# Kernel optimization log

Measured on AMD Instinct MI355X. Metric: run time of the kernel, lower is better.

## Reference

```python
import jax, jax.numpy as jnp
import numpy as np

# --- SOM geometry constants (match init_kwargs) ---
MAP_ROWS, MAP_COLS = 32, 32
N_PROTO = MAP_ROWS * MAP_COLS
SIGMA = 1.0
PBC = True


def _build_neighborhood():
    """Gaussian neighborhood h[i,j]=exp(-dist(i,j)^2/(2*sigma^2)) on a hexagonal
    grid with periodic boundary conditions (faithful to Neighborhoods(...,'Hexagons','grid',PBC=True))."""
    rr, cc = np.meshgrid(np.arange(MAP_ROWS), np.arange(MAP_COLS), indexing='ij')
    # hexagonal lattice coordinates: odd rows shifted by 0.5, row spacing sqrt(3)/2
    x = cc + 0.5 * (rr % 2)
    y = rr * (np.sqrt(3.0) / 2.0)
    pos = np.stack([x.ravel(), y.ravel()], axis=1).astype(np.float64)  # [M, 2]
    diff = pos[:, None, :] - pos[None, :, :]                            # [M, M, 2]
    if PBC:
        width = float(MAP_COLS)
        height = MAP_ROWS * (np.sqrt(3.0) / 2.0)
        d2 = np.full((N_PROTO, N_PROTO), np.inf)
        for sx in (-1.0, 0.0, 1.0):
            for sy in (-1.0, 0.0, 1.0):
                dx = diff[..., 0] + sx * width
                dy = diff[..., 1] + sy * height
                d2 = np.minimum(d2, dx * dx + dy * dy)
    else:
        d2 = (diff ** 2).sum(-1)
    return np.exp(-d2 / (2.0 * SIGMA ** 2)).astype(np.float32)         # [M, M]


H = jnp.asarray(_build_neighborhood())  # constant [M, M] neighborhood matrix


def setup_inputs() -> dict:
    key = jax.random.key(0)
    k1, k2 = jax.random.split(key)
    inputs = jax.random.normal(k1, (16384, 256), dtype=jnp.float32)
    prototypes = jax.random.normal(k2, (N_PROTO, 256), dtype=jnp.float32) * 0.05
    return {"inputs": inputs, "prototypes": prototypes}


def reference(inputs, prototypes):
    # squared euclidean distances d[n, m] = ||x_n - p_m||^2, computed without
    # materializing the (N, M, D) broadcast intermediate
    x2 = jnp.sum(inputs * inputs, axis=1, keepdims=True)        # [N, 1]
    p2 = jnp.sum(prototypes * prototypes, axis=1)               # [M]
    d = x2 - 2.0 * (inputs @ prototypes.T) + p2[None, :]        # [N, M]
    energies = H @ d.T                                          # [M, N]
    bmus = jnp.argmin(energies, axis=0)                         # [N]
    out = 0.5 * jnp.take_along_axis(energies, bmus[None, :], axis=0)  # [1, N]
    return out
```

## Files before the change

### kernel.cpp

```cpp
#include <hip/hip_runtime.h>
#include <hip/hip_bf16.h>
#include <math.h>

#define D 256
#define NPROTO 1024
#define WR 13
#define WC 18
#define WJ (WR * WC)
#define JSUB 59
#define GMAT_BLOCKS (NPROTO / 4)
#define XPREP_BLOCKS (16384 / 8)

#define WAITVM(N) asm volatile("s_waitcnt vmcnt(" #N ")" ::: "memory")

typedef __attribute__((ext_vector_type(8))) short short8;
typedef __attribute__((ext_vector_type(4))) short s16x4;
typedef __attribute__((ext_vector_type(4))) float f32x4;

__device__ __forceinline__ short f2bf(float f) {
    union { __hip_bfloat16 b; short s; } u;
    u.b = __float2bfloat16(f);
    return u.s;
}

__device__ __forceinline__ void gload_lds16(void* lds, const void* g) {
    __builtin_amdgcn_global_load_lds(
        (const __attribute__((address_space(1))) unsigned*)g,
        (__attribute__((address_space(3))) unsigned*)lds, 16, 0, 0);
}

__device__ __forceinline__ void proto_pos(int idx, double& x, double& y) {
    int r = idx >> 5, c = idx & 31;
    x = (double)c + 0.5 * (double)(r & 1);
    y = (double)r * 0.86602540378443864676;
}

__device__ __forceinline__ float hval(int i, int j) {
    double xi, yi, xj, yj;
    proto_pos(i, xi, yi);
    proto_pos(j, xj, yj);
    double dx0 = xi - xj, dy0 = yi - yj;
    const double W = 32.0;
    const double Hh = 27.712812921102035;
    double best = 1e300;
#pragma unroll
    for (int sx = -1; sx <= 1; ++sx) {
        double dx = dx0 + (double)sx * W;
#pragma unroll
        for (int sy = -1; sy <= 1; ++sy) {
            double dy = dy0 + (double)sy * Hh;
            double d2 = dx * dx + dy * dy;
            best = fmin(best, d2);
        }
    }
    return (float)exp(-0.5 * best);
}

__global__ void __launch_bounds__(256) prep_kernel(
    const float* __restrict__ X, const float* __restrict__ P,
    short* __restrict__ Xg, short* __restrict__ Gb,
    float* __restrict__ x2, float* __restrict__ hsum, float* __restrict__ hp2,
    unsigned* __restrict__ out) {
    int t = threadIdx.x;
    int bx = blockIdx.x;

    if (bx >= GMAT_BLOCKS) {
        int row = (bx - GMAT_BLOCKS) * 8 + (t >> 5);
        int g = t & 31;
        const float4* src = reinterpret_cast<const float4*>(X + (size_t)row * D) + g * 2;
        float4 a = src[0], b = src[1];
        float s = a.x * a.x + a.y * a.y + a.z * a.z + a.w * a.w +
                  b.x * b.x + b.y * b.y + b.z * b.z + b.w * b.w;
        s += __shfl_xor(s, 1);
        s += __shfl_xor(s, 2);
        s += __shfl_xor(s, 4);
        s += __shfl_xor(s, 8);
        s += __shfl_xor(s, 16);
        if (g == 0) x2[row] = s;
        short8 w;
        w[0] = f2bf(a.x); w[1] = f2bf(a.y); w[2] = f2bf(a.z); w[3] = f2bf(a.w);
        w[4] = f2bf(b.x); w[5] = f2bf(b.y); w[6] = f2bf(b.z); w[7] = f2bf(b.w);
        int sw = ((g * 8) & 63) ^ ((row & 7) << 3);
        *reinterpret_cast<short8*>(Xg + (size_t)row * D + ((g >> 3) << 6) + sw) = w;
        if (t < 8) out[(bx - GMAT_BLOCKS) * 8 + t] = 0x7f800000u;
        return;
    }

    __shared__ float ht[4][WJ];
    __shared__ int jrow[WJ];
    __shared__ __align__(16) float gpart[4][4][256];
    __shared__ float hqred[4][4];
    __shared__ float hsred[4][4];
    int i0 = bx * 4;
    int r0 = i0 >> 5, c0 = i0 & 31;

    for (int u = t; u < WJ; u += 256) {
        int jr = (r0 + (u / WC) - 6 + 32) & 31;
        int jc = (c0 + (u % WC) - 7 + 32) & 31;
        int j = jr * 32 + jc;
        jrow[u] = j;
#pragma unroll
        for (int s = 0; s < 4; ++s) ht[s][u] = hval(i0 + s, j);
    }
    __syncthreads();

    int w = t >> 6, lane = t & 63;
    int j0 = w * JSUB;
    int j1 = (j0 + JSUB < WJ) ? j0 + JSUB : WJ;
    f32x4 g[4] = {{0.f, 0.f, 0.f, 0.f}, {0.f, 0.f, 0.f, 0.f},
                  {0.f, 0.f, 0.f, 0.f}, {0.f, 0.f, 0.f, 0.f}};
    float hqp[4] = {0.f, 0.f, 0.f, 0.f};
    float hsp[4] = {0.f, 0.f, 0.f, 0.f};
    for (int u = j0; u < j1; ++u) {
        f32x4 pv = *reinterpret_cast<const f32x4*>(P + (size_t)jrow[u] * D + lane * 4);
        float q = pv[0] * pv[0] + pv[1] * pv[1] + pv[2] * pv[2] + pv[3] * pv[3];
#pragma unroll
        for (int s = 0; s < 4; ++s) {
            float h = ht[s][u];
            g[s][0] = fmaf(h, pv[0], g[s][0]);
            g[s][1] = fmaf(h, pv[1], g[s][1]);
            g[s][2] = fmaf(h, pv[2], g[s][2]);
            g[s][3] = fmaf(h, pv[3], g[s][3]);
            hqp[s] = fmaf(h, q, hqp[s]);
            hsp[s] += h;
        }
    }
#pragma unroll
    for (int s = 0; s < 4; ++s)
        *reinterpret_cast<f32x4*>(&gpart[w][s][lane * 4]) = g[s];
#pragma unroll
    for (int s = 0; s < 4; ++s) {
#pragma unroll
        for (int off = 1; off < 64; off <<= 1) hqp[s] += __shfl_xor(hqp[s], off);
    }
    if (lane == 0) {
#pragma unroll
        for (int s = 0; s < 4; ++s) { hqred[w][s] = hqp[s]; hsred[w][s] = hsp[s]; }
    }
    __syncthreads();

    {
        int s = t >> 6;
        f32x4 gs = *reinterpret_cast<const f32x4*>(&gpart[0][s][lane * 4]);
#pragma unroll
        for (int ww = 1; ww < 4; ++ww) {
            f32x4 gp = *reinterpret_cast<const f32x4*>(&gpart[ww][s][lane * 4]);
            gs[0] += gp[0]; gs[1] += gp[1]; gs[2] += gp[2]; gs[3] += gp[3];
        }
        int i = i0 + s;
        s16x4 wv = {f2bf(gs[0]), f2bf(gs[1]), f2bf(gs[2]), f2bf(gs[3])};
        int sw = ((lane * 4) & 63) ^ ((i & 7) << 3);
        *reinterpret_cast<s16x4*>(Gb + (size_t)i * D + ((lane >> 4) << 6) + sw) = wv;
    }
    if (t < 4) {
        hsum[i0 + t] = hsred[0][t] + hsred[1][t] + hsred[2][t] + hsred[3][t];
    } else if (t < 8) {
        int s = t - 4;
        hp2[i0 + s] = hqred[0][s] + hqred[1][s] + hqred[2][s] + hqred[3][s];
    }
}

__global__ void __launch_bounds__(256, 2) som5_kernel(
    const short* __restrict__ Xg, const short* __restrict__ Gb,
    const float* __restrict__ x2, const float* __restrict__ hsum,
    const float* __restrict__ hp2, unsigned* __restrict__ out) {
    __shared__ __align__(16) short Xs[2][128 * 64];
    __shared__ __align__(16) short Gs[2][128 * 64];
    __shared__ float red[2][128];

    const int t = threadIdx.x;
    const int lane = t & 63;
    const int wid = t >> 6;
    const int wr = wid >> 1;
    const int wc = wid & 1;
    const int lm = lane & 15;
    const int lq = lane >> 4;
    const int n0 = blockIdx.x * 128;
    const int ib0 = blockIdx.y * 256;

    f32x4 acc[2][4][4];
#pragma unroll
    for (int it = 0; it < 2; ++it)
#pragma unroll
        for (int m = 0; m < 4; ++m)
#pragma unroll
            for (int n = 0; n < 4; ++n) acc[it][m][n] = (f32x4){0.f, 0.f, 0.f, 0.f};

    auto stage_X = [&](int xb, int kt) {
#pragma unroll
        for (int q = 0; q < 4; ++q) {
            int row = q * 32 + (t >> 3);
            gload_lds16((char*)(&Xs[xb][0]) + q * 4096 + t * 16,
                        Xg + (size_t)(n0 + row) * D + kt * 64 + (t & 7) * 8);
        }
    };
    auto stage_G = [&](int gb, int kt, int it) {
#pragma unroll
        for (int q = 0; q < 4; ++q) {
            int row = q * 32 + (t >> 3);
            gload_lds16((char*)(&Gs[gb][0]) + q * 4096 + t * 16,
                        Gb + (size_t)(ib0 + it * 128 + row) * D + kt * 64 + (t & 7) * 8);
        }
    };

    auto compute = [&](int xb, int gb, int it) {
#pragma unroll
        for (int kk = 0; kk < 2; ++kk) {
            const int off = (kk * 32 + lq * 8) ^ ((lm & 7) << 3);
            short8 a[4], b[4];
#pragma unroll
            for (int m = 0; m < 4; ++m)
                a[m] = *reinterpret_cast<const short8*>(
                    &Xs[xb][(wr * 64 + m * 16 + lm) * 64 + off]);
#pragma unroll
            for (int n = 0; n < 4; ++n)
                b[n] = *reinterpret_cast<const short8*>(
                    &Gs[gb][(wc * 64 + n * 16 + lm) * 64 + off]);
            __builtin_amdgcn_s_setprio(1);
#pragma unroll
            for (int m = 0; m < 4; ++m)
#pragma unroll
                for (int n = 0; n < 4; ++n)
                    acc[it][m][n] = __builtin_amdgcn_mfma_f32_16x16x32_bf16(a[m], b[n], acc[it][m][n], 0, 0, 0);
            __builtin_amdgcn_s_setprio(0);
        }
    };

    stage_G(0, 0, 0);
    stage_X(0, 0);

#pragma unroll
    for (int p = 0; p < 8; ++p) {
        if (p < 7) {
            const int pn = p + 1, ktn = pn >> 1, itn = pn & 1;
            if (itn == 0) stage_X(ktn & 1, ktn);
            stage_G(pn & 1, ktn, itn);
        }
        if (p == 7) { WAITVM(0); }
        else if (p & 1) { WAITVM(8); }
        else { WAITVM(4); }
        __builtin_amdgcn_sched_barrier(0);
        __builtin_amdgcn_s_barrier();
        compute((p >> 1) & 1, p & 1, p & 1);
        __builtin_amdgcn_s_barrier();
    }

    float x2v[4][4];
#pragma unroll
    for (int m = 0; m < 4; ++m)
#pragma unroll
        for (int j = 0; j < 4; ++j)
            x2v[m][j] = x2[n0 + wr * 64 + m * 16 + lq * 4 + j];

    float rmin[4][4];
#pragma unroll
    for (int m = 0; m < 4; ++m)
#pragma unroll
        for (int j = 0; j < 4; ++j) rmin[m][j] = 3.4e38f;

#pragma unroll
    for (int it = 0; it < 2; ++it)
#pragma unroll
        for (int ni = 0; ni < 4; ++ni) {
            int ig = ib0 + it * 128 + wc * 64 + ni * 16 + lm;
            float hs = hsum[ig];
            float hq = hp2[ig];
#pragma unroll
            for (int m = 0; m < 4; ++m)
#pragma unroll
                for (int j = 0; j < 4; ++j) {
                    float e = fmaf(hs, x2v[m][j], hq) - 2.0f * acc[it][m][ni][j];
                    rmin[m][j] = fminf(rmin[m][j], e);
                }
        }

#pragma unroll
    for (int m = 0; m < 4; ++m)
#pragma unroll
        for (int j = 0; j < 4; ++j) {
            float v = rmin[m][j];
            v = fminf(v, __shfl_xor(v, 1));
            v = fminf(v, __shfl_xor(v, 2));
            v = fminf(v, __shfl_xor(v, 4));
            v = fminf(v, __shfl_xor(v, 8));
            rmin[m][j] = v;
        }
    if (lm == 0) {
#pragma unroll
        for (int m = 0; m < 4; ++m)
#pragma unroll
            for (int j = 0; j < 4; ++j)
                red[wc][wr * 64 + m * 16 + lq * 4 + j] = rmin[m][j];
    }
    __syncthreads();
    if (t < 128) {
        float v = fminf(red[0][t], red[1][t]);
        atomicMin(out + n0 + t, __float_as_uint(0.5f * v));
    }
}

extern "C" void kernel_launch(void* const* d_in, const int* in_sizes, int n_in,
                              void* d_out, int out_size, void* d_ws, size_t ws_size,
                              hipStream_t stream) {
    const float* X = (const float*)d_in[0];
    const float* P = (const float*)d_in[1];
    unsigned* out = (unsigned*)d_out;
    int N = in_sizes[0] / D;

    float* ws = (float*)d_ws;
    float* hsum = ws + 1024;
    float* hp2 = ws + 2048;
    float* x2 = ws + 4096;
    short* Gb = (short*)(ws + 32768);
    short* Xg = (short*)(ws + 262144);

    prep_kernel<<<GMAT_BLOCKS + XPREP_BLOCKS, 256, 0, stream>>>(
        X, P, Xg, Gb, x2, hsum, hp2, out);
    som5_kernel<<<dim3(N / 128, NPROTO / 256), 256, 0, stream>>>(
        Xg, Gb, x2, hsum, hp2, out);
}
```

Baseline: 31.97 us.

## Pre-swizzle G into MFMA fragment layout and load B operands directly from global

The prep kernel now writes the bf16 G matrix in a fragment-ordered layout, so each lane can load its MFMA B operand with one 16-byte global load. The main kernel drops the G LDS staging buffer and reads B fragments straight into registers, staging only X through LDS. Each block now covers 128 prototypes instead of 256, which halves the accumulators and doubles the grid. The aim is to cut LDS traffic and barriers and raise occupancy, at the cost of reloading X twice as often across blocks and relying on global-load latency being hidden by the vmcnt waits.

```diff
diff --git a/kernel.cpp b/kernel.cpp
--- a/kernel.cpp
+++ b/kernel.cpp
@@ -14,7 +14,6 @@
 #define WAITVM(N) asm volatile("s_waitcnt vmcnt(" #N ")" ::: "memory")
 
 typedef __attribute__((ext_vector_type(8))) short short8;
-typedef __attribute__((ext_vector_type(4))) short s16x4;
 typedef __attribute__((ext_vector_type(4))) float f32x4;
 
 __device__ __forceinline__ short f2bf(float f) {
@@ -58,7 +57,7 @@
 
 __global__ void __launch_bounds__(256) prep_kernel(
     const float* __restrict__ X, const float* __restrict__ P,
-    short* __restrict__ Xg, short* __restrict__ Gb,
+    short* __restrict__ Xg, short* __restrict__ GbF,
     float* __restrict__ x2, float* __restrict__ hsum, float* __restrict__ hp2,
     unsigned* __restrict__ out) {
     int t = threadIdx.x;
@@ -147,10 +146,22 @@
             f32x4 gp = *reinterpret_cast<const f32x4*>(&gpart[ww][s][lane * 4]);
             gs[0] += gp[0]; gs[1] += gp[1]; gs[2] += gp[2]; gs[3] += gp[3];
         }
-        int i = i0 + s;
-        s16x4 wv = {f2bf(gs[0]), f2bf(gs[1]), f2bf(gs[2]), f2bf(gs[3])};
-        int sw = ((lane * 4) & 63) ^ ((i & 7) << 3);
-        *reinterpret_cast<s16x4*>(Gb + (size_t)i * D + ((lane >> 4) << 6) + sw) = wv;
+        float h0 = __shfl_down(gs[0], 1);
+        float h1 = __shfl_down(gs[1], 1);
+        float h2 = __shfl_down(gs[2], 1);
+        float h3 = __shfl_down(gs[3], 1);
+        if (!(lane & 1)) {
+            int c = lane >> 1;
+            int kg = c >> 2;
+            int q = c & 3;
+            int i = i0 + s;
+            int Ig = i >> 4;
+            short8 wv;
+            wv[0] = f2bf(gs[0]); wv[1] = f2bf(gs[1]); wv[2] = f2bf(gs[2]); wv[3] = f2bf(gs[3]);
+            wv[4] = f2bf(h0);    wv[5] = f2bf(h1);    wv[6] = f2bf(h2);    wv[7] = f2bf(h3);
+            *reinterpret_cast<short8*>(
+                GbF + ((size_t)(Ig * 8 + kg) << 9) + ((i & 15) + 16 * q) * 8) = wv;
+        }
     }
     if (t < 4) {
         hsum[i0 + t] = hsred[0][t] + hsred[1][t] + hsred[2][t] + hsred[3][t];
@@ -160,12 +171,11 @@
     }
 }
 
-__global__ void __launch_bounds__(256, 2) som5_kernel(
-    const short* __restrict__ Xg, const short* __restrict__ Gb,
+__global__ void __launch_bounds__(256) som7_kernel(
+    const short* __restrict__ Xg, const short* __restrict__ GbF,
     const float* __restrict__ x2, const float* __restrict__ hsum,
     const float* __restrict__ hp2, unsigned* __restrict__ out) {
     __shared__ __align__(16) short Xs[2][128 * 64];
-    __shared__ __align__(16) short Gs[2][128 * 64];
     __shared__ float red[2][128];
 
     const int t = threadIdx.x;
@@ -176,15 +186,14 @@
     const int lm = lane & 15;
     const int lq = lane >> 4;
     const int n0 = blockIdx.x * 128;
-    const int ib0 = blockIdx.y * 256;
-
-    f32x4 acc[2][4][4];
-#pragma unroll
-    for (int it = 0; it < 2; ++it)
-#pragma unroll
-        for (int m = 0; m < 4; ++m)
-#pragma unroll
-            for (int n = 0; n < 4; ++n) acc[it][m][n] = (f32x4){0.f, 0.f, 0.f, 0.f};
+    const int ib0 = blockIdx.y * 128;
+    const int Igbase = (ib0 >> 4) + wc * 4;
+
+    f32x4 acc[4][4];
+#pragma unroll
+    for (int m = 0; m < 4; ++m)
+#pragma unroll
+        for (int n = 0; n < 4; ++n) acc[m][n] = (f32x4){0.f, 0.f, 0.f, 0.f};
 
     auto stage_X = [&](int xb, int kt) {
 #pragma unroll
@@ -194,55 +203,57 @@
                         Xg + (size_t)(n0 + row) * D + kt * 64 + (t & 7) * 8);
         }
     };
-    auto stage_G = [&](int gb, int kt, int it) {
-#pragma unroll
-        for (int q = 0; q < 4; ++q) {
-            int row = q * 32 + (t >> 3);
-            gload_lds16((char*)(&Gs[gb][0]) + q * 4096 + t * 16,
-                        Gb + (size_t)(ib0 + it * 128 + row) * D + kt * 64 + (t & 7) * 8);
-        }
-    };
-
-    auto compute = [&](int xb, int gb, int it) {
-#pragma unroll
-        for (int kk = 0; kk < 2; ++kk) {
-            const int off = (kk * 32 + lq * 8) ^ ((lm & 7) << 3);
-            short8 a[4], b[4];
+
+    stage_X(0, 0);
+
+#pragma unroll
+    for (int kt = 0; kt < 4; ++kt) {
+        short8 b0[4], b1[4];
+#pragma unroll
+        for (int n = 0; n < 4; ++n) {
+            const short* fb = GbF + ((size_t)((Igbase + n) * 8 + kt * 2) << 9) + lane * 8;
+            b0[n] = *reinterpret_cast<const short8*>(fb);
+            b1[n] = *reinterpret_cast<const short8*>(fb + 512);
+        }
+        __builtin_amdgcn_sched_barrier(0);
+        if (kt < 3) stage_X((kt + 1) & 1, kt + 1);
+        if (kt < 3) { WAITVM(12); } else { WAITVM(8); }
+        __builtin_amdgcn_sched_barrier(0);
+        __builtin_amdgcn_s_barrier();
+
+        const short* xb = &Xs[kt & 1][0];
+        {
+            const int off = (lq * 8) ^ ((lm & 7) << 3);
+            short8 a[4];
 #pragma unroll
             for (int m = 0; m < 4; ++m)
                 a[m] = *reinterpret_cast<const short8*>(
-                    &Xs[xb][(wr * 64 + m * 16 + lm) * 64 + off]);
-#pragma unroll
-            for (int n = 0; n < 4; ++n)
-                b[n] = *reinterpret_cast<const short8*>(
-                    &Gs[gb][(wc * 64 + n * 16 + lm) * 64 + off]);
+                    &xb[(wr * 64 + m * 16 + lm) * 64 + off]);
+            if (kt < 3) { WAITVM(8); } else { WAITVM(4); }
             __builtin_amdgcn_s_setprio(1);
 #pragma unroll
             for (int m = 0; m < 4; ++m)
 #pragma unroll
                 for (int n = 0; n < 4; ++n)
-                    acc[it][m][n] = __builtin_amdgcn_mfma_f32_16x16x32_bf16(a[m], b[n], acc[it][m][n], 0, 0, 0);
+                    acc[m][n] = __builtin_amdgcn_mfma_f32_16x16x32_bf16(a[m], b0[n], acc[m][n], 0, 0, 0);
             __builtin_amdgcn_s_setprio(0);
         }
-    };
-
-    stage_G(0, 0, 0);
-    stage_X(0, 0);
-
-#pragma unroll
-    for (int p = 0; p < 8; ++p) {
-        if (p < 7) {
-            const int pn = p + 1, ktn = pn >> 1, itn = pn & 1;
-            if (itn == 0) stage_X(ktn & 1, ktn);
-            stage_G(pn & 1, ktn, itn);
-        }
-        if (p == 7) { WAITVM(0); }
-        else if (p & 1) { WAITVM(8); }
-        else { WAITVM(4); }
-        __builtin_amdgcn_sched_barrier(0);
-        __builtin_amdgcn_s_barrier();
-        compute((p >> 1) & 1, p & 1, p & 1);
-        __builtin_amdgcn_s_barrier();
+        {
+            const int off = (32 + lq * 8) ^ ((lm & 7) << 3);
+            short8 a[4];
+#pragma unroll
+            for (int m = 0; m < 4; ++m)
+                a[m] = *reinterpret_cast<const short8*>(
+                    &xb[(wr * 64 + m * 16 + lm) * 64 + off]);
+            if (kt < 3) { WAITVM(4); } else { WAITVM(0); }
+            __builtin_amdgcn_s_setprio(1);
+#pragma unroll
+            for (int m = 0; m < 4; ++m)
+#pragma unroll
+                for (int n = 0; n < 4; ++n)
+                    acc[m][n] = __builtin_amdgcn_mfma_f32_16x16x32_bf16(a[m], b1[n], acc[m][n], 0, 0, 0);
+            __builtin_amdgcn_s_setprio(0);
+        }
     }
 
     float x2v[4][4];
@@ -259,20 +270,18 @@
         for (int j = 0; j < 4; ++j) rmin[m][j] = 3.4e38f;
 
 #pragma unroll
-    for (int it = 0; it < 2; ++it)
-#pragma unroll
-        for (int ni = 0; ni < 4; ++ni) {
-            int ig = ib0 + it * 128 + wc * 64 + ni * 16 + lm;
-            float hs = hsum[ig];
-            float hq = hp2[ig];
-#pragma unroll
-            for (int m = 0; m < 4; ++m)
-#pragma unroll
-                for (int j = 0; j < 4; ++j) {
-                    float e = fmaf(hs, x2v[m][j], hq) - 2.0f * acc[it][m][ni][j];
-                    rmin[m][j] = fminf(rmin[m][j], e);
-                }
-        }
+    for (int ni = 0; ni < 4; ++ni) {
+        int ig = ib0 + wc * 64 + ni * 16 + lm;
+        float hs = hsum[ig];
+        float hq = hp2[ig];
+#pragma unroll
+        for (int m = 0; m < 4; ++m)
+#pragma unroll
+            for (int j = 0; j < 4; ++j) {
+                float e = fmaf(hs, x2v[m][j], hq) - 2.0f * acc[m][ni][j];
+                rmin[m][j] = fminf(rmin[m][j], e);
+            }
+    }
 
 #pragma unroll
     for (int m = 0; m < 4; ++m)
@@ -311,11 +320,11 @@
     float* hsum = ws + 1024;
     float* hp2 = ws + 2048;
     float* x2 = ws + 4096;
-    short* Gb = (short*)(ws + 32768);
+    short* GbF = (short*)(ws + 32768);
     short* Xg = (short*)(ws + 262144);
 
     prep_kernel<<<GMAT_BLOCKS + XPREP_BLOCKS, 256, 0, stream>>>(
-        X, P, Xg, Gb, x2, hsum, hp2, out);
-    som5_kernel<<<dim3(N / 128, NPROTO / 256), 256, 0, stream>>>(
-        Xg, Gb, x2, hsum, hp2, out);
-}
+        X, P, Xg, GbF, x2, hsum, hp2, out);
+    som7_kernel<<<dim3(N / 128, NPROTO / 128), 256, 0, stream>>>(
+        Xg, GbF, x2, hsum, hp2, out);
+}
```

New measurement: 34.58 us. 8.1% more time.
